# Optimization experiments

Hardware: AMD Instinct MI355X
Metric: run time of the kernel (lower is better)

Reference implementation:

```python
import jax, jax.numpy as jnp
import numpy as np

DIM = 256
N_PATCHES = 2048
N_HEADS = 8
BATCH = 2


def setup_inputs() -> dict:
    key = jax.random.key(0)
    ks = jax.random.split(key, 8)
    d = DIM
    s = d ** -0.5
    return {
        "x": jax.random.normal(ks[0], (BATCH, N_PATCHES, d), dtype=jnp.float32),
        # weights stored (in_features, out_features) so y = x @ W + b
        "W_qk": jax.random.normal(ks[1], (d, 2 * d), dtype=jnp.float32) * s,
        "W_v": jax.random.normal(ks[2], (d, d), dtype=jnp.float32) * s,
        "W_proj": jax.random.normal(ks[3], (d, d), dtype=jnp.float32) * s,
        "b_proj": jnp.zeros((d,), dtype=jnp.float32),
        "W_pos": jax.random.normal(ks[4], (2, N_HEADS), dtype=jnp.float32) * 0.5,
        "b_pos": jnp.zeros((N_HEADS,), dtype=jnp.float32),
        "gating": jnp.ones((N_HEADS,), dtype=jnp.float32),
    }


def reference(x, W_qk, W_v, W_proj, b_proj, W_pos, b_pos, gating):
    B, N, C = x.shape
    H = gating.shape[0]
    Dh = C // H
    scale = Dh ** -0.5

    # content attention: q @ k^T softmax
    qk = (x @ W_qk).reshape(B, N, 2, H, Dh)
    q = jnp.transpose(qk[:, :, 0], (0, 2, 1, 3))  # [B,H,N,Dh]
    k = jnp.transpose(qk[:, :, 1], (0, 2, 1, 3))
    patch_score = jax.nn.softmax(jnp.einsum("bhnd,bhmd->bhnm", q, k) * scale, axis=-1)

    # positional attention from relative indices (d, |d|) -> per-head score
    idx = jnp.arange(N, dtype=jnp.float32)
    rel = idx[:, None] - idx[None, :]                      # [N,N]
    rel_feat = jnp.stack([rel, jnp.abs(rel)], axis=-1)     # [N,N,2]
    pos = rel_feat @ W_pos + b_pos                         # [N,N,H]
    pos_score = jax.nn.softmax(jnp.transpose(pos, (2, 0, 1)), axis=-1)  # [H,N,N]

    g = jax.nn.sigmoid(gating)[None, :, None, None]        # [1,H,1,1]
    attn = (1.0 - g) * patch_score + g * pos_score[None]   # [B,H,N,N]
    attn = attn / jnp.sum(attn, axis=-1, keepdims=True)

    v = jnp.transpose((x @ W_v).reshape(B, N, H, Dh), (0, 2, 1, 3))  # [B,H,N,Dh]
    out = jnp.einsum("bhnm,bhmd->bhnd", attn, v)
    out = jnp.transpose(out, (0, 2, 1, 3)).reshape(B, N, C)
    return out @ W_proj + b_proj
```

## Files before the change

kernel.cpp:

```cpp
#include <hip/hip_runtime.h>
#include <hip/hip_bf16.h>
#include <hip/hip_fp16.h>

#define DIM 256
#define NP 2048
#define NH 8
#define BATCH 2
#define DH 32

typedef __attribute__((ext_vector_type(8))) short bshort8;
typedef __attribute__((ext_vector_type(4))) short bshort4;
typedef __attribute__((ext_vector_type(4))) float f32x4;

#define LOG2E 1.44269504f
#define LN2F 0.6931472f
#define QSCALE (0.17677669529663687f * LOG2E)

union U16B { uint4 u; bshort8 s8; bshort4 s4x[2]; __hip_bfloat16 h[8]; };
union U8B  { uint2 u; bshort4 s4; __hip_bfloat16 h[4]; };

__device__ __forceinline__ float fexp2(float x) { return __builtin_amdgcn_exp2f(x); }
__device__ __forceinline__ unsigned packbf(float hi, float lo) {
    return __builtin_amdgcn_perm(__float_as_uint(hi), __float_as_uint(lo), 0x07060302u);
}
__device__ __forceinline__ void gl16(const void* g, void* l) {
    __builtin_amdgcn_global_load_lds(
        (const __attribute__((address_space(1))) void*)g,
        (__attribute__((address_space(3))) void*)l, 16, 0, 0);
}
__device__ __forceinline__ int lds_addr(int row, int colg) {
    return row * 256 + (((colg ^ (row & 7)) & 31) << 3);
}

__global__ __launch_bounds__(256) void prep_kernel(
    const float* __restrict__ Wqk,
    const float* __restrict__ Wv,
    const float* __restrict__ Wproj,
    const float* __restrict__ x,
    __hip_bfloat16* __restrict__ WT,
    __hip_bfloat16* __restrict__ xb) {
    const int t = threadIdx.x;
    const int blk = blockIdx.x;
    if (blk >= 64) {
        const int base = (blk - 64) * 256 + t;
#pragma unroll
        for (int i = 0; i < 16; i++) {
            const int idx = base + i * 16384;
            float4 f = *(const float4*)(x + (size_t)idx * 4);
            U8B a;
            a.h[0] = __float2bfloat16(f.x); a.h[1] = __float2bfloat16(f.y);
            a.h[2] = __float2bfloat16(f.z); a.h[3] = __float2bfloat16(f.w);
            *(uint2*)(xb + (size_t)idx * 4) = a.u;
        }
        return;
    }
    __shared__ float ts[64][65];
    const int ct = blk >> 2, k0 = (blk & 3) * 64;
    const int c0 = ct * 64;
    const float* src; int ldw, cs0; float scl = 1.0f;
    if (ct < 8)       { src = Wqk;   ldw = 512; cs0 = c0;      if (ct < 4) scl = QSCALE; }
    else if (ct < 12) { src = Wv;    ldw = 256; cs0 = c0 - 512; }
    else              { src = Wproj; ldw = 256; cs0 = c0 - 768; }
    const int cc = t & 63, tq = t >> 6;
#pragma unroll
    for (int j = 0; j < 16; j++) {
        int kk = tq * 16 + j;
        ts[kk][cc] = src[(size_t)(k0 + kk) * ldw + cs0 + cc];
    }
    __syncthreads();
    const int kk2 = t & 63;
#pragma unroll
    for (int j = 0; j < 16; j++) {
        int cc2 = tq * 16 + j;
        WT[(size_t)(c0 + cc2) * 256 + k0 + kk2] = __float2bfloat16(ts[kk2][cc2] * scl);
    }
}

__global__ __launch_bounds__(256) void qkv_mfma(
    const __hip_bfloat16* __restrict__ xb,
    const __hip_bfloat16* __restrict__ WT,
    __hip_bfloat16* __restrict__ qT,
    __hip_bfloat16* __restrict__ k,
    __hip_bfloat16* __restrict__ vT) {
    __shared__ __align__(16) __hip_bfloat16 As[64 * 256];
    __shared__ __align__(16) __hip_bfloat16 Bs[64 * 256];
    const int t = threadIdx.x, lane = t & 63, wvid = t >> 6;
    const int l15 = lane & 15, l4 = lane >> 4;
    const int m0 = blockIdx.x * 64;
    const int nb0 = blockIdx.y * 64;
    const int nc = nb0 + wvid * 16 + l15;
    const int lrow = lane >> 5, lcg = lane & 31;

#pragma unroll
    for (int j = 0; j < 8; j++) {
        const int r0 = j * 8 + wvid * 2;
        const int row = r0 + lrow;
        const int cgs = (lcg ^ (row & 7)) & 31;
        gl16(xb + (((size_t)(m0 + row)) << 8) + cgs * 8, (char*)As + r0 * 512);
        gl16(WT + (((size_t)(nb0 + row)) << 8) + cgs * 8, (char*)Bs + r0 * 512);
    }
    __syncthreads();

    f32x4 acc[4] = {{0.f,0.f,0.f,0.f},{0.f,0.f,0.f,0.f},{0.f,0.f,0.f,0.f},{0.f,0.f,0.f,0.f}};
#pragma unroll
    for (int kk = 0; kk < 8; kk++) {
        const int colg = kk * 4 + l4;
        U16B bw; bw.u = *(const uint4*)&Bs[lds_addr(wvid * 16 + l15, colg)];
#pragma unroll
        for (int mt = 0; mt < 4; mt++) {
            U16B ax; ax.u = *(const uint4*)&As[lds_addr(mt * 16 + l15, colg)];
            acc[mt] = __builtin_amdgcn_mfma_f32_16x16x32_bf16(ax.s8, bw.s8, acc[mt], 0, 0, 0);
        }
    }

    if (nb0 < 256) {
        const int b = m0 >> 11;
#pragma unroll
        for (int mt = 0; mt < 4; mt++) {
            int tokn = (m0 & (NP - 1)) + mt * 16 + l4 * 4;
            U8B vv;
#pragma unroll
            for (int r = 0; r < 4; r++) vv.h[r] = __float2bfloat16(acc[mt][r]);
            *(uint2*)(qT + (size_t)(b * 256 + nc) * NP + tokn) = vv.u;
        }
    } else if (nb0 < 512) {
        const int c = nc - 256, h = c >> 5, d = c & 31;
#pragma unroll
        for (int mt = 0; mt < 4; mt++)
#pragma unroll
            for (int r = 0; r < 4; r++) {
                int tok = m0 + mt * 16 + l4 * 4 + r;
                int b = tok >> 11, n = tok & (NP - 1);
                k[((size_t)(b * NH + h) * NP + n) * DH + d] = __float2bfloat16(acc[mt][r]);
            }
    } else {
        const int c = nc - 512;
        const int b = m0 >> 11;
#pragma unroll
        for (int mt = 0; mt < 4; mt++) {
            int tokn = (m0 & (NP - 1)) + mt * 16 + l4 * 4;
            U8B vv;
#pragma unroll
            for (int r = 0; r < 4; r++) vv.h[r] = __float2bfloat16(acc[mt][r]);
            *(uint2*)(vT + (size_t)(b * 256 + c) * NP + tokn) = vv.u;
        }
    }
}

__global__ __launch_bounds__(512, 4) void attn_kernel(
    const __hip_bfloat16* __restrict__ qg,
    const __hip_bfloat16* __restrict__ kg,
    const __hip_bfloat16* __restrict__ vTg,
    const float* __restrict__ Wpos,
    const float* __restrict__ gating,
    __half* __restrict__ NF,
    __half* __restrict__ NB,
    __hip_bfloat16* __restrict__ ao,
    unsigned* __restrict__ sem) {
    __shared__ __align__(16) __hip_bfloat16 Kt[2][2][64][40];
    __shared__ __align__(16) __hip_bfloat16 Vt[2][2][32][72];
    __shared__ float cmb[4][32][16];
    __shared__ float cls[4][16];

    const int t = threadIdx.x;
    const int bid = blockIdx.x;

    if (bid < 64) {
        float* scanL = &cmb[0][0][0];
        float* scanC = scanL + 544;
        const int sbh = bid >> 2, dir = (bid >> 1) & 1, cg = bid & 1;
        const int sh = sbh & (NH - 1), sb = sbh >> 3;
        const int seg = t >> 4, ch16 = t & 15, sch = cg * 16 + ch16;
        const float sw0 = Wpos[sh] * LOG2E, sw1 = Wpos[NH + sh] * LOG2E;
        const float rate = dir ? (sw1 - sw0) : (sw0 + sw1);
        const float mr = fexp2(fminf(rate, 0.f));
        const float mrate = fmaxf(rate, 0.f);
        const int n0 = seg * 64;
        const float dist0 = dir ? (float)(1984 - n0) : (float)n0;
        float sclc = fexp2(-mrate * dist0);
        const float sd8 = fexp2(-mrate * 8.f);
        float sdp[8], mrp[9];
#pragma unroll
        for (int j = 0; j < 8; j++) sdp[j] = fexp2(-mrate * (float)j);
        mrp[0] = 1.f;
#pragma unroll
        for (int j = 1; j < 9; j++) mrp[j] = mrp[j - 1] * mr;
        const float mr8 = mrp[8];
        const __hip_bfloat16* vrow = vTg + ((size_t)(sb * 256 + sh * 32 + sch)) * NP;

        float S[64];
        float F = 0.f;
#pragma unroll
        for (int c = 0; c < 8; c++) {
            U16B vv;
            vv.u = *(const uint4*)(vrow + (dir ? (n0 + 56 - c * 8) : (n0 + c * 8)));
#pragma unroll
            for (int j = 0; j < 8; j++) {
                float V = __bfloat162float(vv.h[dir ? 7 - j : j]);
                float inp = sclc * (sdp[j] * V);
                float Fp = F;
                F = fmaf(mr, F, inp);
                S[c * 8 + j] = dir ? (mr * Fp) : F;
            }
            sclc *= sd8;
        }
        scanL[ch16 * 33 + seg] = F;
        __syncthreads();
        if (t < 16) {
            const float A64 = fexp2(fminf(rate, 0.f) * 64.f);
            float C = 0.f;
            for (int idx = 0; idx < 32; ++idx) {
                const int s = dir ? (31 - idx) : idx;
                scanC[t * 33 + s] = C;
                C = fmaf(A64, C, scanL[t * 33 + s]);
            }
        }
        __syncthreads();
        {
            const float Cin = scanC[ch16 * 33 + seg];
            __half* nout = dir ? NB : NF;
            float cm = Cin;
#pragma unroll
            for (int c = 0; c < 8; c++) {
#pragma unroll
                for (int j = 0; j < 8; j++) {
                    const int i = c * 8 + j;
                    float outv = fmaf(cm, mrp[j + 1], S[i]);
                    const int ni = dir ? (n0 + 63 - i) : (n0 + i);
                    nout[((size_t)sbh * NP + ni) * 32 + sch] = __float2half(outv);
                }
                cm *= mr8;
            }
        }
        __syncthreads();
        if (t == 0) {
            __threadfence();
            __hip_atomic_fetch_add(sem, 1u, __ATOMIC_RELEASE, __HIP_MEMORY_SCOPE_AGENT);
        }
        __syncthreads();
    }

    const int lane = t & 63, wvid = t >> 6;
    const int l15 = lane & 15, l4 = lane >> 4;
    const int qt = wvid & 3, kh = wvid >> 2;
    const int bh = bid >> 5, qb = bid & 31;
    const int h = bh & (NH - 1), b = bh >> 3;
    const int q0 = qb * 64 + qt * 16;
    const int myq = q0 + l15;

    const int st_ = t & 255;
    const int kstart = kh * 1024;
    const __hip_bfloat16* kptr = kg + (size_t)bh * NP * DH + (size_t)(kstart + (st_ >> 2)) * DH + (st_ & 3) * 8;
    const __hip_bfloat16* vptr = vTg + ((size_t)bh * DH + (st_ >> 3)) * NP + kstart + (st_ & 7) * 8;

    const int vd = st_ >> 3, vs = st_ & 7;
    const int vc0 = ((2 * vs) & 3) * 16 + (vs >> 1) * 4;
    const int vc1 = ((2 * vs + 1) & 3) * 16 + (vs >> 1) * 4;

    uint4 kreg = *(const uint4*)kptr;
    uint4 vreg = *(const uint4*)vptr;
    *(uint4*)&Kt[kh][0][st_ >> 2][(st_ & 3) * 8] = kreg;
    *(uint2*)&Vt[kh][0][vd][vc0] = make_uint2(vreg.x, vreg.y);
    *(uint2*)&Vt[kh][0][vd][vc1] = make_uint2(vreg.z, vreg.w);

    const float w0 = Wpos[h] * LOG2E;
    const float w1 = Wpos[NH + h] * LOG2E;
    const float g = 1.0f / (1.0f + __expf(-gating[h]));
    const float nf = (float)myq;

    U16B qv;
#pragma unroll
    for (int j = 0; j < 8; j++)
        qv.h[j] = qg[((size_t)bh * DH + l4 * 8 + j) * NP + myq];

    __syncthreads();

    f32x4 os0 = {0.f,0.f,0.f,0.f}, os1 = {0.f,0.f,0.f,0.f};
    float ls = 0.f;

    for (int it = 0; it < 16; ++it) {
        const int cur = it & 1, nxt = cur ^ 1;

        if (it < 15) {
            kreg = *(const uint4*)(kptr + (size_t)(it + 1) * 64 * DH);
            vreg = *(const uint4*)(vptr + (it + 1) * 64);
        }

        f32x4 st4[4];
#pragma unroll
        for (int kt = 0; kt < 4; kt++) {
            U16B kf; kf.u = *(const uint4*)&Kt[kh][cur][kt * 16 + l15][l4 * 8];
            st4[kt] = __builtin_amdgcn_mfma_f32_16x16x32_bf16(
                kf.s8, qv.s8, (f32x4){0.f,0.f,0.f,0.f}, 0, 0, 0);
        }

        U16B va0, va1, vb0, vb1;
        {
            const __hip_bfloat16* v0 = &Vt[kh][cur][l15][l4 * 16];
            const __hip_bfloat16* v1 = &Vt[kh][cur][16 + l15][l4 * 16];
            va0.u = *(const uint4*)v0;
            va1.u = *(const uint4*)(v0 + 8);
            vb0.u = *(const uint4*)v1;
            vb1.u = *(const uint4*)(v1 + 8);
        }

#pragma unroll
        for (int kt = 0; kt < 4; kt++) {
            const bshort4 fa = (kt < 2) ? va0.s4x[kt & 1] : va1.s4x[kt & 1];
            const bshort4 fb = (kt < 2) ? vb0.s4x[kt & 1] : vb1.s4x[kt & 1];
            float es0 = fexp2(st4[kt][0]), es1 = fexp2(st4[kt][1]);
            float es2 = fexp2(st4[kt][2]), es3 = fexp2(st4[kt][3]);
            ls += (es0 + es1) + (es2 + es3);
            U8B pc;
            pc.u.x = packbf(es1, es0); pc.u.y = packbf(es3, es2);
            os0 = __builtin_amdgcn_mfma_f32_16x16x16bf16_1k(fa, pc.s4, os0, 0, 0, 0);
            os1 = __builtin_amdgcn_mfma_f32_16x16x16bf16_1k(fb, pc.s4, os1, 0, 0, 0);
        }

        if (it < 15) {
            *(uint4*)&Kt[kh][nxt][st_ >> 2][(st_ & 3) * 8] = kreg;
            *(uint2*)&Vt[kh][nxt][vd][vc0] = make_uint2(vreg.x, vreg.y);
            *(uint2*)&Vt[kh][nxt][vd][vc1] = make_uint2(vreg.z, vreg.w);
        }
        __syncthreads();
    }

    ls += __shfl_xor(ls, 16, 64); ls += __shfl_xor(ls, 32, 64);

    if (kh == 1) {
#pragma unroll
        for (int r = 0; r < 4; r++) {
            cmb[qt][l4 * 4 + r][l15]      = os0[r];
            cmb[qt][16 + l4 * 4 + r][l15] = os1[r];
        }
        if (l4 == 0) cls[qt][l15] = ls;
    }
    if (t == 0) {
        while (__hip_atomic_load(sem, __ATOMIC_ACQUIRE, __HIP_MEMORY_SCOPE_AGENT) < 64u)
            __builtin_amdgcn_s_sleep(2);
        __threadfence();
    }
    __syncthreads();
    if (kh == 0) {
        ls += cls[qt][l15];
        const float cs = (1.0f - g) / ls;
        const float a2 = w0 + w1, b2 = w1 - w0;
        const float pmF = fmaxf(0.f, a2 * nf);
        const float pmB = fmaxf(0.f, b2 * (2047.f - nf));
        const float pm  = fmaxf(pmF, pmB);
        const float eF = fexp2(pmF - pm);
        const float eB = fexp2(pmB - pm);
        const float aa = fabsf(a2), ab = fabsf(b2);
        const float Mf = 2047.f - nf;
        const float lpFv = (aa > 1e-9f)
            ? expm1f(-LN2F * aa * (nf + 1.f)) / expm1f(-LN2F * aa)
            : (nf + 1.f);
        float lpBv;
        if (ab > 1e-9f) {
            const float E = expm1f(-LN2F * ab * Mf) / expm1f(-LN2F * ab);
            lpBv = (b2 > 0.f) ? E : fexp2(-ab) * E;
        } else lpBv = Mf;
        const float lpv = eF * lpFv + eB * lpBv;
        const float cp = g / lpv;
        const size_t lpi = (size_t)bh * NP + myq;
        const __half* nfp = NF + lpi * 32 + l4 * 4;
        const __half* nbp = NB + lpi * 32 + l4 * 4;
        const size_t orow = ((size_t)b * NP + myq) * DIM + h * DH;
        U8B o0, o1;
#pragma unroll
        for (int r = 0; r < 4; r++) {
            float p0 = eF * __half2float(nfp[r])      + eB * __half2float(nbp[r]);
            float p1 = eF * __half2float(nfp[16 + r]) + eB * __half2float(nbp[16 + r]);
            o0.h[r] = __float2bfloat16(cs * (os0[r] + cmb[qt][l4 * 4 + r][l15]) + cp * p0);
            o1.h[r] = __float2bfloat16(cs * (os1[r] + cmb[qt][16 + l4 * 4 + r][l15]) + cp * p1);
        }
        *(uint2*)(ao + orow + l4 * 4)      = o0.u;
        *(uint2*)(ao + orow + 16 + l4 * 4) = o1.u;
    }
}

__global__ __launch_bounds__(256) void proj_mfma(
    const __hip_bfloat16* __restrict__ ao,
    const __hip_bfloat16* __restrict__ WT,
    const float* __restrict__ bias,
    float* __restrict__ out) {
    __shared__ __align__(16) __hip_bfloat16 As[64 * 256];
    __shared__ __align__(16) __hip_bfloat16 Bs[64 * 256];
    const int t = threadIdx.x, lane = t & 63, wvid = t >> 6;
    const int l15 = lane & 15, l4 = lane >> 4;
    const int m0 = blockIdx.x * 64;
    const int nb0 = blockIdx.y * 64;
    const int nc = nb0 + wvid * 16 + l15;
    const int lrow = lane >> 5, lcg = lane & 31;

#pragma unroll
    for (int j = 0; j < 8; j++) {
        const int r0 = j * 8 + wvid * 2;
        const int row = r0 + lrow;
        const int cgs = (lcg ^ (row & 7)) & 31;
        gl16(ao + (((size_t)(m0 + row)) << 8) + cgs * 8, (char*)As + r0 * 512);
        gl16(WT + (((size_t)(768 + nb0 + row)) << 8) + cgs * 8, (char*)Bs + r0 * 512);
    }
    __syncthreads();

    f32x4 acc[4] = {{0.f,0.f,0.f,0.f},{0.f,0.f,0.f,0.f},{0.f,0.f,0.f,0.f},{0.f,0.f,0.f,0.f}};
#pragma unroll
    for (int kk = 0; kk < 8; kk++) {
        const int colg = kk * 4 + l4;
        U16B bw; bw.u = *(const uint4*)&Bs[lds_addr(wvid * 16 + l15, colg)];
#pragma unroll
        for (int mt = 0; mt < 4; mt++) {
            U16B ax; ax.u = *(const uint4*)&As[lds_addr(mt * 16 + l15, colg)];
            acc[mt] = __builtin_amdgcn_mfma_f32_16x16x32_bf16(ax.s8, bw.s8, acc[mt], 0, 0, 0);
        }
    }

    const float bb = bias[nc];
#pragma unroll
    for (int mt = 0; mt < 4; mt++)
#pragma unroll
        for (int r = 0; r < 4; r++) {
            int tok = m0 + mt * 16 + l4 * 4 + r;
            out[(size_t)tok * 256 + nc] = acc[mt][r] + bb;
        }
}

extern "C" void kernel_launch(void* const* d_in, const int* in_sizes, int n_in,
                              void* d_out, int out_size, void* d_ws, size_t ws_size,
                              hipStream_t stream) {
    const float* x      = (const float*)d_in[0];
    const float* Wqk    = (const float*)d_in[1];
    const float* Wv     = (const float*)d_in[2];
    const float* Wproj  = (const float*)d_in[3];
    const float* bproj  = (const float*)d_in[4];
    const float* Wpos   = (const float*)d_in[5];
    const float* gating = (const float*)d_in[7];
    float* out = (float*)d_out;

    char* w = (char*)d_ws;
    __hip_bfloat16* WT = (__hip_bfloat16*)w;
    __hip_bfloat16* qT = WT + 262144;
    __hip_bfloat16* k  = qT + 1048576;
    __hip_bfloat16* vT = k  + 1048576;
    __hip_bfloat16* ao = vT + 1048576;
    __hip_bfloat16* xb = ao + 1048576;
    __half* NF = (__half*)(w + 11010048);
    __half* NB = (__half*)(w + 13107200);
    unsigned* sem = (unsigned*)(w + (16u << 20));

    hipMemsetAsync(sem, 0, 64, stream);

    prep_kernel<<<128, 256, 0, stream>>>(Wqk, Wv, Wproj, x, WT, xb);
    qkv_mfma<<<dim3(64, 12), 256, 0, stream>>>(xb, WT, qT, k, vT);
    attn_kernel<<<BATCH * NH * (NP / 64), 512, 0, stream>>>(qT, k, vT, Wpos, gating,
                                                            NF, NB, ao, sem);
    proj_mfma<<<dim3(64, 4), 256, 0, stream>>>(ao, WT, bproj, out);
}
```

Measured before the change: 125.0 us.

## Recompute positional scan in second pass and store NF/NB channel-major vectorized

```diff
diff --git a/kernel.cpp b/kernel.cpp
--- a/kernel.cpp
+++ b/kernel.cpp
@@ -18,6 +18,7 @@
 
 union U16B { uint4 u; bshort8 s8; bshort4 s4x[2]; __hip_bfloat16 h[8]; };
 union U8B  { uint2 u; bshort4 s4; __hip_bfloat16 h[4]; };
+union UH8  { uint4 u; ushort s[8]; };
 
 __device__ __forceinline__ float fexp2(float x) { return __builtin_amdgcn_exp2f(x); }
 __device__ __forceinline__ unsigned packbf(float hi, float lo) {
@@ -38,9 +39,11 @@
     const float* __restrict__ Wproj,
     const float* __restrict__ x,
     __hip_bfloat16* __restrict__ WT,
-    __hip_bfloat16* __restrict__ xb) {
+    __hip_bfloat16* __restrict__ xb,
+    unsigned* __restrict__ sem) {
     const int t = threadIdx.x;
     const int blk = blockIdx.x;
+    if (blk == 0 && t == 0) *sem = 0;
     if (blk >= 64) {
         const int base = (blk - 64) * 256 + t;
 #pragma unroll
@@ -177,34 +180,28 @@
         const float mrate = fmaxf(rate, 0.f);
         const int n0 = seg * 64;
         const float dist0 = dir ? (float)(1984 - n0) : (float)n0;
-        float sclc = fexp2(-mrate * dist0);
+        const float scl0 = fexp2(-mrate * dist0);
         const float sd8 = fexp2(-mrate * 8.f);
-        float sdp[8], mrp[9];
+        float sdp[8];
 #pragma unroll
         for (int j = 0; j < 8; j++) sdp[j] = fexp2(-mrate * (float)j);
-        mrp[0] = 1.f;
-#pragma unroll
-        for (int j = 1; j < 9; j++) mrp[j] = mrp[j - 1] * mr;
-        const float mr8 = mrp[8];
         const __hip_bfloat16* vrow = vTg + ((size_t)(sb * 256 + sh * 32 + sch)) * NP;
 
-        float S[64];
-        float F = 0.f;
-#pragma unroll
-        for (int c = 0; c < 8; c++) {
-            U16B vv;
-            vv.u = *(const uint4*)(vrow + (dir ? (n0 + 56 - c * 8) : (n0 + c * 8)));
-#pragma unroll
-            for (int j = 0; j < 8; j++) {
-                float V = __bfloat162float(vv.h[dir ? 7 - j : j]);
-                float inp = sclc * (sdp[j] * V);
-                float Fp = F;
-                F = fmaf(mr, F, inp);
-                S[c * 8 + j] = dir ? (mr * Fp) : F;
+        {
+            float F = 0.f, sclc = scl0;
+#pragma unroll
+            for (int c = 0; c < 8; c++) {
+                U16B vv;
+                vv.u = *(const uint4*)(vrow + (dir ? (n0 + 56 - c * 8) : (n0 + c * 8)));
+#pragma unroll
+                for (int j = 0; j < 8; j++) {
+                    float V = __bfloat162float(vv.h[dir ? 7 - j : j]);
+                    F = fmaf(mr, F, sclc * (sdp[j] * V));
+                }
+                sclc *= sd8;
             }
-            sclc *= sd8;
-        }
-        scanL[ch16 * 33 + seg] = F;
+            scanL[ch16 * 33 + seg] = F;
+        }
         __syncthreads();
         if (t < 16) {
             const float A64 = fexp2(fminf(rate, 0.f) * 64.f);
@@ -217,19 +214,24 @@
         }
         __syncthreads();
         {
-            const float Cin = scanC[ch16 * 33 + seg];
-            __half* nout = dir ? NB : NF;
-            float cm = Cin;
+            float Fc = scanC[ch16 * 33 + seg];
+            float sclc = scl0;
+            __half* nout = (dir ? NB : NF) + ((size_t)sbh * 32 + sch) * NP;
 #pragma unroll
             for (int c = 0; c < 8; c++) {
+                const int tokb = dir ? (n0 + 56 - c * 8) : (n0 + c * 8);
+                U16B vv; vv.u = *(const uint4*)(vrow + tokb);
+                UH8 ob;
 #pragma unroll
                 for (int j = 0; j < 8; j++) {
-                    const int i = c * 8 + j;
-                    float outv = fmaf(cm, mrp[j + 1], S[i]);
-                    const int ni = dir ? (n0 + 63 - i) : (n0 + i);
-                    nout[((size_t)sbh * NP + ni) * 32 + sch] = __float2half(outv);
+                    float V = __bfloat162float(vv.h[dir ? 7 - j : j]);
+                    float tt = sclc * (sdp[j] * V);
+                    Fc = fmaf(mr, Fc, tt);
+                    float outv = dir ? (Fc - tt) : Fc;
+                    ob.s[dir ? 7 - j : j] = __half_as_ushort(__float2half(outv));
                 }
-                cm *= mr8;
+                *(uint4*)(nout + tokb) = ob.u;
+                sclc *= sd8;
             }
         }
         __syncthreads();
@@ -362,15 +364,16 @@
         } else lpBv = Mf;
         const float lpv = eF * lpFv + eB * lpBv;
         const float cp = g / lpv;
-        const size_t lpi = (size_t)bh * NP + myq;
-        const __half* nfp = NF + lpi * 32 + l4 * 4;
-        const __half* nbp = NB + lpi * 32 + l4 * 4;
+        const __half* nfb = NF + (size_t)bh * 32 * NP + myq;
+        const __half* nbb = NB + (size_t)bh * 32 * NP + myq;
         const size_t orow = ((size_t)b * NP + myq) * DIM + h * DH;
         U8B o0, o1;
 #pragma unroll
         for (int r = 0; r < 4; r++) {
-            float p0 = eF * __half2float(nfp[r])      + eB * __half2float(nbp[r]);
-            float p1 = eF * __half2float(nfp[16 + r]) + eB * __half2float(nbp[16 + r]);
+            const size_t c0i = (size_t)(l4 * 4 + r) * NP;
+            const size_t c1i = (size_t)(16 + l4 * 4 + r) * NP;
+            float p0 = eF * __half2float(nfb[c0i]) + eB * __half2float(nbb[c0i]);
+            float p1 = eF * __half2float(nfb[c1i]) + eB * __half2float(nbb[c1i]);
             o0.h[r] = __float2bfloat16(cs * (os0[r] + cmb[qt][l4 * 4 + r][l15]) + cp * p0);
             o1.h[r] = __float2bfloat16(cs * (os1[r] + cmb[qt][16 + l4 * 4 + r][l15]) + cp * p1);
         }
@@ -448,9 +451,7 @@
     __half* NB = (__half*)(w + 13107200);
     unsigned* sem = (unsigned*)(w + (16u << 20));
 
-    hipMemsetAsync(sem, 0, 64, stream);
-
-    prep_kernel<<<128, 256, 0, stream>>>(Wqk, Wv, Wproj, x, WT, xb);
+    prep_kernel<<<128, 256, 0, stream>>>(Wqk, Wv, Wproj, x, WT, xb, sem);
     qkv_mfma<<<dim3(64, 12), 256, 0, stream>>>(xb, WT, qT, k, vT);
     attn_kernel<<<BATCH * NH * (NP / 64), 512, 0, stream>>>(qT, k, vT, Wpos, gating,
                                                             NF, NB, ao, sem);
```

Result: slower. 222.7 us (+78.1%).
